# Kernel optimization log

Hardware: AMD Instinct MI355X
Metric: run time of the kernel (lower is better)

The kernel has to match this reference:

```python
import jax, jax.numpy as jnp
import numpy as np


def _sq_cdist(x, y):
    # x: [B,N,D], y: [B,M,D] -> squared L2 distances [B,N,M]
    x_norm = jnp.sum(x * x, axis=-1, keepdims=True)          # [B,N,1]
    y_norm = jnp.sum(y * y, axis=-1, keepdims=True)          # [B,M,1]
    xy = jnp.einsum('bnd,bmd->bnm', x, y)                    # [B,N,M]
    return x_norm - 2.0 * xy + jnp.swapaxes(y_norm, -2, -1)  # [B,N,M]


def setup_inputs() -> dict:
    key = jax.random.key(0)
    kx, ky = jax.random.split(key)
    B, N, M, D = 8, 8192, 8192, 3
    x = jax.random.normal(kx, (B, N, D), dtype=jnp.float32)
    y = jax.random.normal(ky, (B, M, D), dtype=jnp.float32)
    return {"x": x, "y": y}


def reference(x, y):
    d = _sq_cdist(x, y)  # [B,N,M] squared distances (no sqrt, matching original)
    # original d was [B,M,N]; min(dim=2)->per-y-point min over N, min(dim=1)->per-x-point min over M
    per_y = jnp.min(d, axis=1)  # [B,M]
    per_x = jnp.min(d, axis=2)  # [B,N]
    return jnp.mean(per_y) + jnp.mean(per_x)
```

## Files before the change

### kernel.cpp

```cpp
#include <hip/hip_runtime.h>
#include <math.h>


#define B_      8
#define N_      8192
#define Q_      8
#define S_      16
#define CHUNK_  (N_ / S_)


__global__ __launch_bounds__(256)
void minpass_kernel(const float* __restrict__ x, const float* __restrict__ y,
                    float* __restrict__ partX, float* __restrict__ partY) {
    __shared__ float4 sq[CHUNK_];

    const int b    = blockIdx.y;
    const int z    = blockIdx.z;
    const int pass = z >> 4;
    const int s    = z & (S_ - 1);

    const float* qpts = pass ? y : x;
    const float* tpts = pass ? x : y;
    float*       part = pass ? partY : partX;

    {
        const float* p = tpts + ((long)b * N_ + s * CHUNK_) * 3 + 6 * threadIdx.x;
        float a0 = p[0], a1 = p[1], a2 = p[2];
        float a3 = p[3], a4 = p[4], a5 = p[5];
        sq[2 * threadIdx.x + 0] = make_float4(-2.0f * a0, -2.0f * a1, -2.0f * a2,
                                              fmaf(a0, a0, fmaf(a1, a1, a2 * a2)));
        sq[2 * threadIdx.x + 1] = make_float4(-2.0f * a3, -2.0f * a4, -2.0f * a5,
                                              fmaf(a3, a3, fmaf(a4, a4, a5 * a5)));
    }
    __syncthreads();

    const int iq0 = (blockIdx.x * blockDim.x + threadIdx.x) * Q_;
    const float4* qp4 = (const float4*)(qpts + ((long)b * N_ + iq0) * 3);
    float qx[Q_], qy[Q_], qz[Q_];
    {
        const float4 f0 = qp4[0], f1 = qp4[1], f2 = qp4[2];
        const float4 f3 = qp4[3], f4 = qp4[4], f5 = qp4[5];
        qx[0]=f0.x; qy[0]=f0.y; qz[0]=f0.z;
        qx[1]=f0.w; qy[1]=f1.x; qz[1]=f1.y;
        qx[2]=f1.z; qy[2]=f1.w; qz[2]=f2.x;
        qx[3]=f2.y; qy[3]=f2.z; qz[3]=f2.w;
        qx[4]=f3.x; qy[4]=f3.y; qz[4]=f3.z;
        qx[5]=f3.w; qy[5]=f4.x; qz[5]=f4.y;
        qx[6]=f4.z; qy[6]=f4.w; qz[6]=f5.x;
        qx[7]=f5.y; qy[7]=f5.z; qz[7]=f5.w;
    }

    float m[Q_];
#pragma unroll
    for (int i = 0; i < Q_; ++i) m[i] = __builtin_inff();

    for (int j = 0; j < CHUNK_; j += 8) {
        float4 t[8];
#pragma unroll
        for (int k = 0; k < 8; ++k) t[k] = sq[j + k];
#pragma unroll
        for (int i = 0; i < Q_; ++i) {
            float s0 = fmaf(qx[i], t[0].x, fmaf(qy[i], t[0].y, fmaf(qz[i], t[0].z, t[0].w)));
            float s1 = fmaf(qx[i], t[1].x, fmaf(qy[i], t[1].y, fmaf(qz[i], t[1].z, t[1].w)));
            float s2 = fmaf(qx[i], t[2].x, fmaf(qy[i], t[2].y, fmaf(qz[i], t[2].z, t[2].w)));
            float s3 = fmaf(qx[i], t[3].x, fmaf(qy[i], t[3].y, fmaf(qz[i], t[3].z, t[3].w)));
            float s4 = fmaf(qx[i], t[4].x, fmaf(qy[i], t[4].y, fmaf(qz[i], t[4].z, t[4].w)));
            float s5 = fmaf(qx[i], t[5].x, fmaf(qy[i], t[5].y, fmaf(qz[i], t[5].z, t[5].w)));
            float s6 = fmaf(qx[i], t[6].x, fmaf(qy[i], t[6].y, fmaf(qz[i], t[6].z, t[6].w)));
            float s7 = fmaf(qx[i], t[7].x, fmaf(qy[i], t[7].y, fmaf(qz[i], t[7].z, t[7].w)));
            float u0 = fminf(fminf(s0, s1), s2);
            float u1 = fminf(fminf(s3, s4), s5);
            float u2 = fminf(fminf(s6, s7), u0);
            m[i]     = fminf(fminf(u1, u2), m[i]);
        }
    }

    float r[Q_];
#pragma unroll
    for (int i = 0; i < Q_; ++i) {
        float xn = fmaf(qx[i], qx[i], fmaf(qy[i], qy[i], qz[i] * qz[i]));
        r[i] = fmaxf(m[i] + xn, 0.0f);
    }
    float* dst = part + (long)s * (B_ * N_) + (long)b * N_ + iq0;
    *(float4*)(dst + 0) = make_float4(r[0], r[1], r[2], r[3]);
    *(float4*)(dst + 4) = make_float4(r[4], r[5], r[6], r[7]);
}

__global__ __launch_bounds__(256)
void merge_kernel(const float* __restrict__ partX, const float* __restrict__ partY,
                  float* __restrict__ bsum, int BN) {
    const int g = blockIdx.x * blockDim.x + threadIdx.x;
    const float* base = (g < BN) ? (partX + g) : (partY + (g - BN));

    float m = __builtin_inff();
#pragma unroll
    for (int s = 0; s < S_; ++s)
        m = fminf(m, base[(long)s * BN]);

    for (int off = 32; off > 0; off >>= 1)
        m += __shfl_down(m, off, 64);
    __shared__ float wsum[4];
    const int lane = threadIdx.x & 63;
    const int w    = threadIdx.x >> 6;
    if (lane == 0) wsum[w] = m;
    __syncthreads();
    if (threadIdx.x == 0)
        bsum[blockIdx.x] = (wsum[0] + wsum[1]) + (wsum[2] + wsum[3]);
}

__global__ __launch_bounds__(64)
void final_kernel(const float* __restrict__ bsum, float* __restrict__ out,
                  int nb, float scale) {
    float s = 0.0f;
    for (int k = threadIdx.x; k < nb; k += 64)
        s += bsum[k];
    for (int off = 32; off > 0; off >>= 1)
        s += __shfl_down(s, off, 64);
    if (threadIdx.x == 0) out[0] = s * scale;
}

extern "C" void kernel_launch(void* const* d_in, const int* in_sizes, int n_in,
                              void* d_out, int out_size, void* d_ws, size_t ws_size,
                              hipStream_t stream) {
    const float* x = (const float*)d_in[0];
    const float* y = (const float*)d_in[1];
    float* out = (float*)d_out;

    const int BN = B_ * N_;

    float* partX = (float*)d_ws;
    float* partY = partX + (size_t)S_ * BN;
    float* bsum  = partY + (size_t)S_ * BN;

    minpass_kernel<<<dim3(N_ / (256 * Q_), B_, 2 * S_), 256, 0, stream>>>(x, y, partX, partY);

    const int nb = 2 * BN / 256;
    merge_kernel<<<nb, 256, 0, stream>>>(partX, partY, bsum, BN);
    final_kernel<<<1, 64, 0, stream>>>(bsum, out, nb, 1.0f / 65536.0f);
}
```

Measured before the change: 135.6 us.

## Precompute target quads in a prep kernel and stream them from global with register double-buffering

```diff
diff --git a/kernel.cpp b/kernel.cpp
--- a/kernel.cpp
+++ b/kernel.cpp
@@ -9,30 +9,35 @@
 #define CHUNK_  (N_ / S_)
 
 
+__global__ void prep_kernel(const float* __restrict__ x, const float* __restrict__ y,
+                            float4* __restrict__ quadX, float4* __restrict__ quadY,
+                            int BN, int BM) {
+    int i = blockIdx.x * blockDim.x + threadIdx.x;
+    if (i >= BN + BM) return;
+    const float* src;
+    float4* dst;
+    int k;
+    if (i < BN) { src = x; dst = quadX; k = i; }
+    else        { src = y; dst = quadY; k = i - BN; }
+    float a0 = src[3 * k + 0];
+    float a1 = src[3 * k + 1];
+    float a2 = src[3 * k + 2];
+    dst[k] = make_float4(-2.0f * a0, -2.0f * a1, -2.0f * a2,
+                         fmaf(a0, a0, fmaf(a1, a1, a2 * a2)));
+}
+
 __global__ __launch_bounds__(256)
 void minpass_kernel(const float* __restrict__ x, const float* __restrict__ y,
+                    const float4* __restrict__ quadX, const float4* __restrict__ quadY,
                     float* __restrict__ partX, float* __restrict__ partY) {
-    __shared__ float4 sq[CHUNK_];
-
     const int b    = blockIdx.y;
     const int z    = blockIdx.z;
     const int pass = z >> 4;
     const int s    = z & (S_ - 1);
 
-    const float* qpts = pass ? y : x;
-    const float* tpts = pass ? x : y;
-    float*       part = pass ? partY : partX;
-
-    {
-        const float* p = tpts + ((long)b * N_ + s * CHUNK_) * 3 + 6 * threadIdx.x;
-        float a0 = p[0], a1 = p[1], a2 = p[2];
-        float a3 = p[3], a4 = p[4], a5 = p[5];
-        sq[2 * threadIdx.x + 0] = make_float4(-2.0f * a0, -2.0f * a1, -2.0f * a2,
-                                              fmaf(a0, a0, fmaf(a1, a1, a2 * a2)));
-        sq[2 * threadIdx.x + 1] = make_float4(-2.0f * a3, -2.0f * a4, -2.0f * a5,
-                                              fmaf(a3, a3, fmaf(a4, a4, a5 * a5)));
-    }
-    __syncthreads();
+    const float*  qpts = pass ? y : x;
+    const float4* tq   = pass ? quadX : quadY;
+    float*        part = pass ? partY : partX;
 
     const int iq0 = (blockIdx.x * blockDim.x + threadIdx.x) * Q_;
     const float4* qp4 = (const float4*)(qpts + ((long)b * N_ + iq0) * 3);
@@ -50,30 +55,44 @@
         qx[7]=f5.y; qy[7]=f5.z; qz[7]=f5.w;
     }
 
+    const float4* base = tq + (long)b * N_ + s * CHUNK_;
+
     float m[Q_];
 #pragma unroll
     for (int i = 0; i < Q_; ++i) m[i] = __builtin_inff();
 
-    for (int j = 0; j < CHUNK_; j += 8) {
-        float4 t[8];
+#define COMPUTE(T)                                                                     \
+    {                                                                                  \
+        _Pragma("unroll")                                                              \
+        for (int i = 0; i < Q_; ++i) {                                                 \
+            float s0 = fmaf(qx[i], T[0].x, fmaf(qy[i], T[0].y, fmaf(qz[i], T[0].z, T[0].w))); \
+            float s1 = fmaf(qx[i], T[1].x, fmaf(qy[i], T[1].y, fmaf(qz[i], T[1].z, T[1].w))); \
+            float s2 = fmaf(qx[i], T[2].x, fmaf(qy[i], T[2].y, fmaf(qz[i], T[2].z, T[2].w))); \
+            float s3 = fmaf(qx[i], T[3].x, fmaf(qy[i], T[3].y, fmaf(qz[i], T[3].z, T[3].w))); \
+            float s4 = fmaf(qx[i], T[4].x, fmaf(qy[i], T[4].y, fmaf(qz[i], T[4].z, T[4].w))); \
+            float s5 = fmaf(qx[i], T[5].x, fmaf(qy[i], T[5].y, fmaf(qz[i], T[5].z, T[5].w))); \
+            float s6 = fmaf(qx[i], T[6].x, fmaf(qy[i], T[6].y, fmaf(qz[i], T[6].z, T[6].w))); \
+            float s7 = fmaf(qx[i], T[7].x, fmaf(qy[i], T[7].y, fmaf(qz[i], T[7].z, T[7].w))); \
+            float u0 = fminf(fminf(s0, s1), s2);                           \
+            float u1 = fminf(fminf(s3, s4), s5);                           \
+            float u2 = fminf(fminf(s6, s7), u0);                           \
+            m[i]     = fminf(fminf(u1, u2), m[i]);                         \
+        }                                                                              \
+    }
+
+    float4 ta[8], tb[8];
 #pragma unroll
-        for (int k = 0; k < 8; ++k) t[k] = sq[j + k];
+    for (int k = 0; k < 8; ++k) ta[k] = base[k];
+
+    for (int j = 0; j < CHUNK_; j += 16) {
 #pragma unroll
-        for (int i = 0; i < Q_; ++i) {
-            float s0 = fmaf(qx[i], t[0].x, fmaf(qy[i], t[0].y, fmaf(qz[i], t[0].z, t[0].w)));
-            float s1 = fmaf(qx[i], t[1].x, fmaf(qy[i], t[1].y, fmaf(qz[i], t[1].z, t[1].w)));
-            float s2 = fmaf(qx[i], t[2].x, fmaf(qy[i], t[2].y, fmaf(qz[i], t[2].z, t[2].w)));
-            float s3 = fmaf(qx[i], t[3].x, fmaf(qy[i], t[3].y, fmaf(qz[i], t[3].z, t[3].w)));
-            float s4 = fmaf(qx[i], t[4].x, fmaf(qy[i], t[4].y, fmaf(qz[i], t[4].z, t[4].w)));
-            float s5 = fmaf(qx[i], t[5].x, fmaf(qy[i], t[5].y, fmaf(qz[i], t[5].z, t[5].w)));
-            float s6 = fmaf(qx[i], t[6].x, fmaf(qy[i], t[6].y, fmaf(qz[i], t[6].z, t[6].w)));
-            float s7 = fmaf(qx[i], t[7].x, fmaf(qy[i], t[7].y, fmaf(qz[i], t[7].z, t[7].w)));
-            float u0 = fminf(fminf(s0, s1), s2);
-            float u1 = fminf(fminf(s3, s4), s5);
-            float u2 = fminf(fminf(s6, s7), u0);
-            m[i]     = fminf(fminf(u1, u2), m[i]);
-        }
+        for (int k = 0; k < 8; ++k) tb[k] = base[j + 8 + k];
+        COMPUTE(ta)
+#pragma unroll
+        for (int k = 0; k < 8; ++k) ta[k] = base[j + 16 + k];
+        COMPUTE(tb)
     }
+#undef COMPUTE
 
     float r[Q_];
 #pragma unroll
@@ -128,11 +147,16 @@
 
     const int BN = B_ * N_;
 
-    float* partX = (float*)d_ws;
-    float* partY = partX + (size_t)S_ * BN;
-    float* bsum  = partY + (size_t)S_ * BN;
+    float4* quadX = (float4*)d_ws;
+    float4* quadY = quadX + BN;
+    float*  partX = (float*)(quadY + BN);
+    float*  partY = partX + (size_t)S_ * BN;
+    float*  bsum  = partY + (size_t)S_ * BN;
 
-    minpass_kernel<<<dim3(N_ / (256 * Q_), B_, 2 * S_), 256, 0, stream>>>(x, y, partX, partY);
+    prep_kernel<<<(2 * BN + 255) / 256, 256, 0, stream>>>(x, y, quadX, quadY, BN, BN);
+
+    minpass_kernel<<<dim3(N_ / (256 * Q_), B_, 2 * S_), 256, 0, stream>>>(
+        x, y, quadX, quadY, partX, partY);
 
     const int nb = 2 * BN / 256;
     merge_kernel<<<nb, 256, 0, stream>>>(partX, partY, bsum, BN);
```

Measured after the change: 167.2 us. 23.3% more time.
